# Optimization experiments

Measured on AMD Instinct MI355X. Metric: run time of the kernel, lower is better.

Reference implementation:

```python
import jax, jax.numpy as jnp
import numpy as np

# 17 predefined bone groups indexing into the 16 bones (ragged sizes 2/3/4)
LIMBS = [[0, 1, 2], [3, 4, 5], [6, 7], [8, 9], [10, 11, 12], [13, 14, 15],
         [6, 7, 1, 2], [6, 7, 4, 5], [6, 7, 11, 12], [6, 7, 14, 15], [6, 7, 9],
         [14, 15, 11, 12], [1, 2, 4, 5], [14, 15, 4, 5], [11, 12, 4, 5],
         [10, 0], [13, 3]]
N_GROUPS = 17
MAXL = 4          # max group size; ragged groups padded to this
C = 3             # xyz coordinates per bone
HIDDEN = 16       # mlp_hidden_dim default


def _padded_indices():
    idx = np.zeros((N_GROUPS, MAXL), np.int32)
    rowmask = np.zeros((N_GROUPS, MAXL * C), np.float32)  # mask over flattened (limb, coord)
    for g, limbs in enumerate(LIMBS):
        idx[g, :len(limbs)] = limbs
        rowmask[g, :len(limbs) * C] = 1.0
    return idx, rowmask


def setup_inputs() -> dict:
    key = jax.random.key(0)
    k_x, k_w1, k_b1, k_w2, k_b2 = jax.random.split(key, 5)
    B, T = 2048, 243
    x = jax.random.normal(k_x, (B, T, 16, C), dtype=jnp.float32)
    idx_np, rowmask_np = _padded_indices()
    # per-group MLP params, stacked over the 17 groups
    W1 = jax.random.normal(k_w1, (N_GROUPS, MAXL * C, HIDDEN), jnp.float32) * 0.1
    # zero the weight rows that correspond to padded (absent) limbs ->
    # identical math to the original ragged per-group Linear(n*3, hidden)
    W1 = W1 * jnp.asarray(rowmask_np)[:, :, None]
    b1 = jax.random.normal(k_b1, (N_GROUPS, HIDDEN), jnp.float32) * 0.1
    W2 = jax.random.normal(k_w2, (N_GROUPS, HIDDEN, C), jnp.float32) * 0.1
    b2 = jax.random.normal(k_b2, (N_GROUPS, C), jnp.float32) * 0.1
    return {"x": x, "W1": W1, "b1": b1, "W2": W2, "b2": b2,
            "idx": jnp.asarray(idx_np)}


def reference(x, W1, b1, W2, b2, idx):
    B, T, J, Cc = x.shape
    # gather all 17 groups at once: [B, T, 17, MAXL, C]
    g = x[:, :, idx, :]
    g = g.reshape(B, T, N_GROUPS, MAXL * Cc)        # flatten limbs*coords per group
    # batched small GEMMs across the 17 groups (fused per-group BoneMLP)
    h = jax.nn.relu(jnp.einsum('btgi,gih->btgh', g, W1) + b1)  # [B,T,17,HIDDEN]
    out = jnp.einsum('btgh,ghc->btgc', h, W2) + b2             # [B,T,17,3]
    return out
```

## Files before the change

kernel.cpp:

```cpp
#include <hip/hip_runtime.h>


#define NG   17
#define MAXL 4

static constexpr int KL[NG][MAXL] = {
    {0,1,2,0},   {3,4,5,0},   {6,7,0,0},   {8,9,0,0},
    {10,11,12,0},{13,14,15,0},{6,7,1,2},   {6,7,4,5},
    {6,7,11,12}, {6,7,14,15}, {6,7,9,0},   {14,15,11,12},
    {1,2,4,5},   {14,15,4,5}, {11,12,4,5}, {10,0,0,0},
    {13,3,0,0}
};

__global__ __launch_bounds__(256)
void bone_kernel(const float* __restrict__ x,
                 const float* __restrict__ W1,
                 const float* __restrict__ b1,
                 const float* __restrict__ W2,
                 const float* __restrict__ b2,
                 float* __restrict__ out)
{
    const long long pos = (long long)blockIdx.x * 256 + threadIdx.x;

    const float4* xin = reinterpret_cast<const float4*>(x + pos * 48);
    float xr[48];
    #pragma unroll
    for (int i = 0; i < 12; ++i) {
        const float4 v = xin[i];
        xr[i * 4 + 0] = v.x;
        xr[i * 4 + 1] = v.y;
        xr[i * 4 + 2] = v.z;
        xr[i * 4 + 3] = v.w;
    }

    float* o = out + pos * 51;

    #pragma unroll
    for (int g = 0; g < NG; ++g) {
        float h[16];
        #pragma unroll
        for (int j = 0; j < 16; ++j) h[j] = b1[g * 16 + j];

        #pragma unroll
        for (int s = 0; s < MAXL; ++s) {
            const int limb = KL[g][s];
            #pragma unroll
            for (int c = 0; c < 3; ++c) {
                const float xv = xr[limb * 3 + c];
                const int   i  = s * 3 + c;
                #pragma unroll
                for (int j = 0; j < 16; ++j)
                    h[j] = fmaf(xv, W1[g * 192 + i * 16 + j], h[j]);
            }
        }
        #pragma unroll
        for (int j = 0; j < 16; ++j) h[j] = fmaxf(h[j], 0.0f);

        #pragma unroll
        for (int c = 0; c < 3; ++c) {
            float acc = b2[g * 3 + c];
            #pragma unroll
            for (int j = 0; j < 16; ++j)
                acc = fmaf(h[j], W2[g * 48 + j * 3 + c], acc);
            o[g * 3 + c] = acc;
        }
    }
}

extern "C" void kernel_launch(void* const* d_in, const int* in_sizes, int n_in,
                              void* d_out, int out_size, void* d_ws, size_t ws_size,
                              hipStream_t stream)
{
    const float* x  = (const float*)d_in[0];
    const float* W1 = (const float*)d_in[1];
    const float* b1 = (const float*)d_in[2];
    const float* W2 = (const float*)d_in[3];
    const float* b2 = (const float*)d_in[4];
    float* out = (float*)d_out;

    bone_kernel<<<1944, 256, 0, stream>>>(x, W1, b1, W2, b2, out);
}
```

Measured before the change: 307.7 us.

## Stage outputs through LDS in three group chunks for coalesced stores

The 17 groups are computed in three chunks. Each chunk's per-thread outputs are written transposed into a padded LDS buffer, then read back so consecutive threads write consecutive output addresses, replacing the strided 51-float-per-thread stores. Launch bounds now request 6 blocks per CU to constrain register use. This adds barriers and LDS traffic, and the tighter register budget may cause spills given the 48-float input array.

Result: slower. 345.7 us (+12.4%).

```diff
diff --git a/kernel.cpp b/kernel.cpp
--- a/kernel.cpp
+++ b/kernel.cpp
@@ -3,6 +3,7 @@
 
 #define NG   17
 #define MAXL 4
+#define PITCH 257
 
 static constexpr int KL[NG][MAXL] = {
     {0,1,2,0},   {3,4,5,0},   {6,7,0,0},   {8,9,0,0},
@@ -12,7 +13,9 @@
     {13,3,0,0}
 };
 
-__global__ __launch_bounds__(256)
+static constexpr int CB[4] = {0, 6, 12, 17};
+
+__global__ __launch_bounds__(256, 6)
 void bone_kernel(const float* __restrict__ x,
                  const float* __restrict__ W1,
                  const float* __restrict__ b1,
@@ -20,9 +23,11 @@
                  const float* __restrict__ b2,
                  float* __restrict__ out)
 {
-    const long long pos = (long long)blockIdx.x * 256 + threadIdx.x;
+    __shared__ float lds[18 * PITCH];
+    const int tid = threadIdx.x;
+    const long long blk = blockIdx.x;
 
-    const float4* xin = reinterpret_cast<const float4*>(x + pos * 48);
+    const float4* xin = reinterpret_cast<const float4*>(x + (blk * 256 + tid) * 48LL);
     float xr[48];
     #pragma unroll
     for (int i = 0; i < 12; ++i) {
@@ -33,37 +38,54 @@
         xr[i * 4 + 3] = v.w;
     }
 
-    float* o = out + pos * 51;
+    float* o = out + blk * (256LL * 51);
 
     #pragma unroll
-    for (int g = 0; g < NG; ++g) {
-        float h[16];
-        #pragma unroll
-        for (int j = 0; j < 16; ++j) h[j] = b1[g * 16 + j];
+    for (int c = 0; c < 3; ++c) {
+        const int g0 = CB[c], g1 = CB[c + 1];
+        const int e0 = g0 * 3;
+        const int E  = (g1 - g0) * 3;
 
         #pragma unroll
-        for (int s = 0; s < MAXL; ++s) {
-            const int limb = KL[g][s];
+        for (int g = g0; g < g1; ++g) {
+            float h[16];
             #pragma unroll
-            for (int c = 0; c < 3; ++c) {
-                const float xv = xr[limb * 3 + c];
-                const int   i  = s * 3 + c;
+            for (int j = 0; j < 16; ++j) h[j] = b1[g * 16 + j];
+
+            #pragma unroll
+            for (int s = 0; s < MAXL; ++s) {
+                const int limb = KL[g][s];
+                #pragma unroll
+                for (int cc = 0; cc < 3; ++cc) {
+                    const float xv = xr[limb * 3 + cc];
+                    const int   i  = s * 3 + cc;
+                    #pragma unroll
+                    for (int j = 0; j < 16; ++j)
+                        h[j] = fmaf(xv, W1[g * 192 + i * 16 + j], h[j]);
+                }
+            }
+            #pragma unroll
+            for (int j = 0; j < 16; ++j) h[j] = fmaxf(h[j], 0.0f);
+
+            #pragma unroll
+            for (int cc = 0; cc < 3; ++cc) {
+                float acc = b2[g * 3 + cc];
                 #pragma unroll
                 for (int j = 0; j < 16; ++j)
-                    h[j] = fmaf(xv, W1[g * 192 + i * 16 + j], h[j]);
+                    acc = fmaf(h[j], W2[g * 48 + j * 3 + cc], acc);
+                lds[(g * 3 + cc - e0) * PITCH + tid] = acc;
             }
         }
-        #pragma unroll
-        for (int j = 0; j < 16; ++j) h[j] = fmaxf(h[j], 0.0f);
+        __syncthreads();
 
         #pragma unroll
-        for (int c = 0; c < 3; ++c) {
-            float acc = b2[g * 3 + c];
-            #pragma unroll
-            for (int j = 0; j < 16; ++j)
-                acc = fmaf(h[j], W2[g * 48 + j * 3 + c], acc);
-            o[g * 3 + c] = acc;
+        for (int it = 0; it < E; ++it) {
+            const int f   = it * 256 + tid;
+            const int pos = f / E;
+            const int e   = f - pos * E;
+            o[pos * 51 + e0 + e] = lds[e * PITCH + pos];
         }
+        if (c < 2) __syncthreads();
     }
 }
 
```
